# Performance work log

Measured on AMD Instinct MI355X. Metric: run time of the kernel, lower is better.

Reference implementation:

```python
import jax, jax.numpy as jnp
import numpy as np

N = 6144      # nodes
DIN = 65      # input_dim (1 time + 64 space coords)
DOUT = 65     # output_dim per head
H = 4         # nheads
EPS = 1e-7
MIN = 1e-15
# curvature c = 1 throughout (MultiHeadGraphAttentionLayer hardcodes curvature=1)

def arcosh(z):
    return jnp.log(z + jnp.sqrt(jnp.maximum(z * z - 1.0, 0.0)))

def hyp_proj(u):
    # project onto hyperboloid: recompute time coord
    y = u[..., 1:]
    t = jnp.sqrt(1.0 + jnp.sum(y * y, -1, keepdims=True))
    return jnp.concatenate([t, y], -1)

def expmap0(u):
    v = u[..., 1:]
    n = jnp.maximum(jnp.linalg.norm(v, axis=-1, keepdims=True), MIN)
    return jnp.concatenate([jnp.cosh(n), jnp.sinh(n) * v / n], -1)

def logmap0(x):
    y = x[..., 1:]
    n = jnp.maximum(jnp.linalg.norm(y, axis=-1, keepdims=True), MIN)
    t = jnp.maximum(x[..., :1], 1.0 + EPS)
    return jnp.concatenate([jnp.zeros_like(t), arcosh(t) * y / n], -1)

def hyp_linear(x, W):
    # HypLinear (use_bias=False, eval mode): mobius_matvec = exp0(log0(x) @ W^T), then proj
    return hyp_proj(expmap0(logmap0(x) @ W.T))

def to_poincare(x):
    return x[..., 1:] / (x[..., :1] + 1.0)

def to_hyperboloid(p):
    s = jnp.sum(p * p, -1, keepdims=True)
    return jnp.concatenate([1.0 + s, 2.0 * p], -1) / jnp.maximum(1.0 - s, MIN)

def mobius_half(v):
    # 0.5 (x) v  (mobius scalar multiplication, c=1)
    n = jnp.maximum(jnp.linalg.norm(v, axis=-1, keepdims=True), MIN)
    return jnp.tanh(0.5 * jnp.arctanh(jnp.minimum(n, 1.0 - EPS))) * v / n

def head(x, adj_t, Wa, Wd, Wo):
    att = hyp_linear(x, Wa)   # [N, DOUT]
    red = hyp_linear(x, Wd)   # [N, DOUT]
    # pairwise hyperboloid sqdist via Minkowski inner product (negate time coord)
    am = att.at[:, 0].multiply(-1.0)
    theta = jnp.maximum(-(am @ att.T), 1.0 + EPS)          # [N, N]
    S = jnp.minimum(arcosh(theta) ** 2, 50.0)
    # coef[i, j] = -adj[j, i] * sqdist for incoming edges (mask = adj^T)
    coef = jnp.where(adj_t > 0.01, -adj_t * S, 0.0)
    # F.normalize along incoming-edge axis (zeros don't change the L2 norm)
    a = coef / jnp.maximum(jnp.linalg.norm(coef, axis=-1, keepdims=True), 1e-12)
    pv = to_poincare(red)                                   # [N, DOUT-1]
    lam = 2.0 / jnp.maximum(1.0 - jnp.sum(pv * pv, -1), MIN)  # conformal factors [N]
    num = (a * lam[None, :]) @ pv                           # [N, DOUT-1]
    den = jnp.sum(jnp.abs(a) * (lam - 1.0)[None, :], -1, keepdims=True)
    m = mobius_half(num / jnp.maximum(den, MIN))            # mobius midpoint
    return hyp_linear(to_hyperboloid(m), Wo)                # [N, DOUT]

def reference(x, adj, W_att, W_data, W_out, W_lin):
    adj_t = adj.T
    hs = jnp.stack([head(x, adj_t, W_att[h], W_data[h], W_out[h]) for h in range(H)], axis=1)  # [N, H, DOUT]
    p = to_poincare(hs).reshape(x.shape[0], -1)             # PoincareBall.concat -> [N, H*(DOUT-1)]
    return hyp_linear(to_hyperboloid(p), W_lin)             # [N, H*DOUT]

def setup_inputs():
    key = jax.random.key(0)
    ks = jax.random.split(key, 8)
    sp = 0.1 * jax.random.normal(ks[0], (N, DIN - 1), jnp.float32)
    x = jnp.concatenate([jnp.sqrt(1.0 + jnp.sum(sp * sp, -1, keepdims=True)), sp], -1)
    adj = (jax.random.uniform(ks[1], (N, N)) < 32.0 / N).astype(jnp.float32)
    adj = jnp.maximum(adj, jnp.eye(N, dtype=jnp.float32))  # every node >=1 incoming edge
    def xavier(k, shape):
        b = (6.0 / (shape[0] + shape[1])) ** 0.5
        return jax.random.uniform(k, shape, jnp.float32, -b, b)
    W_att = jnp.stack([xavier(jax.random.fold_in(ks[2], h), (DOUT, DIN)) for h in range(H)])
    W_data = jnp.stack([xavier(jax.random.fold_in(ks[3], h), (DOUT, DIN)) for h in range(H)])
    W_out = jnp.stack([xavier(jax.random.fold_in(ks[4], h), (DOUT, DOUT)) for h in range(H)])
    W_lin = xavier(ks[5], (H * DOUT, H * (DOUT - 1) + 1))
    return {"x": x, "adj": adj, "W_att": W_att, "W_data": W_data, "W_out": W_out, "W_lin": W_lin}
```

## Files before the change

### kernel.cpp

```cpp
#include <hip/hip_runtime.h>
#include <math.h>

#define N 6144
#define H 4
#define CAP 128
#define MINF 1e-15f
#define ONE_EPS  1.0000001192092896f
#define ONE_MEPS 0.9999998807907104f

__device__ __forceinline__ float wave_reduce_sum(float v) {
    v += __shfl_xor(v, 32, 64);
    v += __shfl_xor(v, 16, 64);
    v += __shfl_xor(v, 8, 64);
    v += __shfl_xor(v, 4, 64);
    v += __shfl_xor(v, 2, 64);
    v += __shfl_xor(v, 1, 64);
    return v;
}

__device__ __forceinline__ float arcosh_f(float z) {
    return logf(z + sqrtf(fmaxf(z * z - 1.0f, 0.0f)));
}

__global__ void k_prep(const float* __restrict__ x, float* __restrict__ lmv,
                       const float* __restrict__ W_att, const float* __restrict__ W_data,
                       const float* __restrict__ W_out,
                       float* __restrict__ Bp, float* __restrict__ Bo,
                       int* __restrict__ cnt) {
    int b = blockIdx.x;
    if (b < 1536) {
        int i = b * 4 + (threadIdx.x >> 6);
        int lane = threadIdx.x & 63;
        float y = x[i * 65 + 1 + lane];
        float ss = wave_reduce_sum(y * y);
        float n = fmaxf(sqrtf(ss), MINF);
        float t = fmaxf(x[i * 65], ONE_EPS);
        lmv[i * 64 + lane] = arcosh_f(t) * y / n;
    } else if (b < 1728) {
        int tid = (b - 1536) * 256 + threadIdx.x;
        int m = tid >> 12;
        int r = tid & 4095;
        int k = r >> 6, o = r & 63;
        const float* src;
        if (m < 4) src = W_att + m * 65 * 65;
        else if (m < 8) src = W_data + (m - 4) * 65 * 65;
        else src = W_out + (m - 8) * 65 * 65;
        float val = src[(1 + o) * 65 + (1 + k)];
        if (m < 8) Bp[m * 4096 + k * 64 + o] = val;
        else Bo[(m - 8) * 4096 + k * 64 + o] = val;
    } else {
        cnt[(b - 1728) * 256 + threadIdx.x] = 0;
    }
}

__global__ void k_build_csr(const float* __restrict__ adj,
                            int* __restrict__ cnt, int* __restrict__ idx) {
    const unsigned total4 = (unsigned)N * N / 4;
    const float4* a4 = (const float4*)adj;
    for (unsigned e = blockIdx.x * blockDim.x + threadIdx.x; e < total4;
         e += gridDim.x * blockDim.x) {
        float4 v = a4[e];
        unsigned base = e * 4u;
        float vals[4] = {v.x, v.y, v.z, v.w};
        #pragma unroll
        for (int q = 0; q < 4; q++) {
            if (vals[q] > 0.01f) {
                unsigned t = base + q;
                int j = t / N;
                int i = t % N;
                int pos = atomicAdd(&cnt[i], 1);
                if (pos < CAP) idx[i * CAP + pos] = j;
            }
        }
    }
}

__global__ void k_gemm64(const float* __restrict__ A, size_t aStrideY,
                         const float* __restrict__ Bp, float* __restrict__ C, int ldc) {
    __shared__ float As[16][64];
    __shared__ float Bs[16][64];
    const float* Ab = A + aStrideY * blockIdx.y;
    const float* Bb = Bp + (size_t)blockIdx.y * 4096;
    int i0 = blockIdx.x * 64;
    int ocol = blockIdx.y * 64;
    int tid = threadIdx.x;
    int tx = tid & 15, ty = tid >> 4;
    float acc[4][4] = {};
    for (int k0 = 0; k0 < 64; k0 += 16) {
        {
            int mm = tid >> 2, kq = tid & 3;
            float4 v = *(const float4*)(Ab + (size_t)(i0 + mm) * 64 + k0 + kq * 4);
            As[kq * 4 + 0][mm] = v.x;
            As[kq * 4 + 1][mm] = v.y;
            As[kq * 4 + 2][mm] = v.z;
            As[kq * 4 + 3][mm] = v.w;
        }
        {
            int kk = tid >> 4, o4 = tid & 15;
            float4 bvv = *(const float4*)(Bb + (k0 + kk) * 64 + o4 * 4);
            *(float4*)&Bs[kk][o4 * 4] = bvv;
        }
        __syncthreads();
        #pragma unroll
        for (int kk = 0; kk < 16; kk++) {
            float4 av = *(const float4*)&As[kk][ty * 4];
            float4 bv = *(const float4*)&Bs[kk][tx * 4];
            float a[4] = {av.x, av.y, av.z, av.w};
            float b[4] = {bv.x, bv.y, bv.z, bv.w};
            #pragma unroll
            for (int r = 0; r < 4; r++)
                #pragma unroll
                for (int c = 0; c < 4; c++) acc[r][c] += a[r] * b[c];
        }
        __syncthreads();
    }
    #pragma unroll
    for (int r = 0; r < 4; r++) {
        int i = i0 + ty * 4 + r;
        #pragma unroll
        for (int c = 0; c < 4; c++)
            C[(size_t)i * ldc + ocol + tx * 4 + c] = acc[r][c];
    }
}

__global__ void k_head_epi(const float* __restrict__ UAUD,
                           float* __restrict__ attv, float2* __restrict__ a0l,
                           float* __restrict__ pv) {
    int i = blockIdx.x;
    int t = threadIdx.x;
    int h = t >> 6, lane = t & 63;
    float ua = UAUD[(size_t)i * 512 + t];
    float ud = UAUD[(size_t)i * 512 + 256 + t];
    float na = fmaxf(sqrtf(wave_reduce_sum(ua * ua)), MINF);
    float sha = sinhf(na);
    attv[((size_t)h * N + i) * 64 + lane] = sha * ua / na;
    float nd = fmaxf(sqrtf(wave_reduce_sum(ud * ud)), MINF);
    float shd = sinhf(nd), chd = coshf(nd);
    float pvd = (shd * ud / nd) / (chd + 1.0f);
    pv[((size_t)h * N + i) * 64 + lane] = pvd;
    float sp = wave_reduce_sum(pvd * pvd);
    if (lane == 0) {
        a0l[h * N + i] = make_float2(coshf(na), 2.0f / fmaxf(1.0f - sp, MINF));
    }
}

__global__ void __launch_bounds__(256) k_attn(
        const int* __restrict__ cnt, const int* __restrict__ idx,
        const float* __restrict__ attv, const float2* __restrict__ a0l,
        const float* __restrict__ pv, float* __restrict__ lm2) {
    __shared__ float wls[4][CAP];
    __shared__ int jls[4][CAP];
    int w = threadIdx.x >> 6, lane = threadIdx.x & 63;
    int i = blockIdx.x * 4 + w;
    int h = blockIdx.y;
    const float* attvh = attv + (size_t)h * N * 64;
    const float* pvh = pv + (size_t)h * N * 64;
    const float2* a0lh = a0l + (size_t)h * N;

    int c = lane & 3;
    float4 aireg[4];
    #pragma unroll
    for (int q = 0; q < 4; q++)
        aireg[q] = *(const float4*)(attvh + (size_t)i * 64 + q * 16 + c * 4);
    float ai0 = a0lh[i].x;
    int nn = min(cnt[i], CAP);

    float accd = 0.f, accss = 0.f;
    for (int base = 0; base < nn; base += 16) {
        int t = base + (lane >> 2);
        bool act = t < nn;
        int j = act ? idx[i * CAP + t] : i;
        float2 al = a0lh[j];
        float d = 0.f;
        #pragma unroll
        for (int q = 0; q < 4; q++) {
            float4 b = *(const float4*)(attvh + (size_t)j * 64 + q * 16 + c * 4);
            float4 a = aireg[q];
            d += a.x * b.x + a.y * b.y + a.z * b.z + a.w * b.w;
        }
        d += __shfl_xor(d, 1, 64);
        d += __shfl_xor(d, 2, 64);
        float theta = fmaxf(ai0 * al.x - d, ONE_EPS);
        float ar = arcosh_f(theta);
        float S = fminf(ar * ar, 50.0f);
        if (!act) S = 0.f;
        if (c == 0) {
            accd += S * (al.y - 1.0f);
            accss += S * S;
            wls[w][t] = S * al.y;
            jls[w][t] = j;
        }
    }
    accd = wave_reduce_sum(accd);
    accss = wave_reduce_sum(accss);
    float nrm = fmaxf(sqrtf(accss), 1e-12f);
    float den = fmaxf(accd / nrm, MINF);
    float scl = 1.0f / (nrm * den);

    float accn = 0.f;
    #pragma unroll 4
    for (int t = 0; t < nn; t++) {
        int j = jls[w][t];
        float wq = wls[w][t];
        accn = fmaf(wq, pvh[(size_t)j * 64 + lane], accn);
    }
    float v = -scl * accn;
    float nv = fmaxf(sqrtf(wave_reduce_sum(v * v)), MINF);
    float nc = fminf(nv, ONE_MEPS);
    float mh = tanhf(0.5f * atanhf(nc));
    float md = mh * v / nv;
    float s = wave_reduce_sum(md * md);
    float Dh = fmaxf(1.0f - s, MINF);
    float hb0 = (1.0f + s) / Dh;
    float hbv = 2.0f * md / Dh;
    float nh = fmaxf(2.0f * sqrtf(s) / Dh, MINF);
    float t2 = fmaxf(hb0, ONE_EPS);
    lm2[((size_t)h * N + i) * 64 + lane] = arcosh_f(t2) * hbv / nh;
}

__global__ void k_out_epi(const float* __restrict__ u2, float* __restrict__ lmF) {
    __shared__ float part[4];
    int i = blockIdx.x;
    int t = threadIdx.x;
    int w = t >> 6;
    float u = u2[(size_t)i * 256 + t];
    float nv = fmaxf(sqrtf(wave_reduce_sum(u * u)), MINF);
    float sh = sinhf(nv), ch = coshf(nv);
    float pd = (sh * u / nv) / (ch + 1.0f);
    float ss = wave_reduce_sum(pd * pd);
    if ((t & 63) == 0) part[w] = ss;
    __syncthreads();
    float s = part[0] + part[1] + part[2] + part[3];
    float Dh = fmaxf(1.0f - s, MINF);
    float hb0 = (1.0f + s) / Dh;
    float hbv = 2.0f * pd / Dh;
    float n = fmaxf(2.0f * sqrtf(s) / Dh, MINF);
    float tt = fmaxf(hb0, ONE_EPS);
    lmF[(size_t)i * 256 + t] = arcosh_f(tt) * hbv / n;
}

__global__ void k_final_gemm(const float* __restrict__ A,
                             const float* __restrict__ Wl,
                             float* __restrict__ U) {
    __shared__ float As[16][64];
    __shared__ float Bs[16][64];
    int i0 = blockIdx.x * 64;
    int o0 = blockIdx.y * 64;
    int tid = threadIdx.x;
    int tx = tid & 15, ty = tid >> 4;
    float acc[4][4] = {};
    for (int k0 = 0; k0 < 256; k0 += 16) {
        {
            int mm = tid >> 2;
            int kq = tid & 3;
            const float4 v = *(const float4*)(A + (size_t)(i0 + mm) * 256 + k0 + kq * 4);
            As[kq * 4 + 0][mm] = v.x;
            As[kq * 4 + 1][mm] = v.y;
            As[kq * 4 + 2][mm] = v.z;
            As[kq * 4 + 3][mm] = v.w;
        }
        {
            int oo = tid >> 2;
            int kq = tid & 3;
            int o = o0 + oo;
            if (o < 259) {
                const float* src = Wl + (size_t)(1 + o) * 257 + 1 + k0 + kq * 4;
                Bs[kq * 4 + 0][oo] = src[0];
                Bs[kq * 4 + 1][oo] = src[1];
                Bs[kq * 4 + 2][oo] = src[2];
                Bs[kq * 4 + 3][oo] = src[3];
            } else {
                Bs[kq * 4 + 0][oo] = 0.f;
                Bs[kq * 4 + 1][oo] = 0.f;
                Bs[kq * 4 + 2][oo] = 0.f;
                Bs[kq * 4 + 3][oo] = 0.f;
            }
        }
        __syncthreads();
        #pragma unroll
        for (int kk = 0; kk < 16; kk++) {
            float4 av = *(const float4*)&As[kk][ty * 4];
            float4 bv = *(const float4*)&Bs[kk][tx * 4];
            float a[4] = {av.x, av.y, av.z, av.w};
            float b[4] = {bv.x, bv.y, bv.z, bv.w};
            #pragma unroll
            for (int r = 0; r < 4; r++)
                #pragma unroll
                for (int c = 0; c < 4; c++) acc[r][c] += a[r] * b[c];
        }
        __syncthreads();
    }
    #pragma unroll
    for (int r = 0; r < 4; r++) {
        int i = i0 + ty * 4 + r;
        #pragma unroll
        for (int c = 0; c < 4; c++) {
            int o = o0 + tx * 4 + c;
            if (o < 259) U[(size_t)i * 260 + o] = acc[r][c];
        }
    }
}

__global__ void k_final_epilogue(const float* __restrict__ U, float* __restrict__ out) {
    __shared__ float part[4];
    int i = blockIdx.x;
    int t = threadIdx.x;
    float a = U[(size_t)i * 260 + t];
    float b = (t < 3) ? U[(size_t)i * 260 + 256 + t] : 0.f;
    float ss = wave_reduce_sum(a * a + b * b);
    if ((t & 63) == 0) part[t >> 6] = ss;
    __syncthreads();
    ss = part[0] + part[1] + part[2] + part[3];
    float nv = fmaxf(sqrtf(ss), MINF);
    float sh = sinhf(nv);
    float scale = sh / nv;
    out[(size_t)i * 260 + 1 + t] = scale * a;
    if (t < 3) out[(size_t)i * 260 + 257 + t] = scale * b;
    if (t == 0) out[(size_t)i * 260] = sqrtf(1.0f + sh * sh);
}

extern "C" void kernel_launch(void* const* d_in, const int* in_sizes, int n_in,
                              void* d_out, int out_size, void* d_ws, size_t ws_size,
                              hipStream_t stream) {
    const float* x = (const float*)d_in[0];
    const float* adj = (const float*)d_in[1];
    const float* W_att = (const float*)d_in[2];
    const float* W_data = (const float*)d_in[3];
    const float* W_out = (const float*)d_in[4];
    const float* W_lin = (const float*)d_in[5];
    float* out = (float*)d_out;

    char* ws = (char*)d_ws;
    size_t off = 0;
    auto alloc = [&](size_t bytes) {
        void* ptr = ws + off;
        off += (bytes + 255) & ~(size_t)255;
        return ptr;
    };
    int* cnt = (int*)alloc((size_t)N * 4);
    int* idx = (int*)alloc((size_t)N * CAP * 4);
    float* lmv = (float*)alloc((size_t)N * 64 * 4);
    float* UAUD = (float*)alloc((size_t)N * 512 * 4);
    float* attv = (float*)alloc((size_t)H * N * 64 * 4);
    float2* a0l = (float2*)alloc((size_t)H * N * 8);
    float* pvb = (float*)alloc((size_t)H * N * 64 * 4);
    float* lm2 = (float*)alloc((size_t)H * N * 64 * 4);
    float* Bp = (float*)alloc((size_t)8 * 4096 * 4);
    float* Bo = (float*)alloc((size_t)4 * 4096 * 4);
    float* U = UAUD;
    float* lmF = attv;
    float* u2 = pvb;

    k_prep<<<1752, 256, 0, stream>>>(x, lmv, W_att, W_data, W_out, Bp, Bo, cnt);
    k_build_csr<<<4096, 256, 0, stream>>>(adj, cnt, idx);
    k_gemm64<<<dim3(N / 64, 8), 256, 0, stream>>>(lmv, 0, Bp, UAUD, 512);
    k_head_epi<<<N, 256, 0, stream>>>(UAUD, attv, a0l, pvb);
    k_attn<<<dim3(N / 4, H), 256, 0, stream>>>(cnt, idx, attv, a0l, pvb, lm2);
    k_gemm64<<<dim3(N / 64, 4), 256, 0, stream>>>(lm2, (size_t)N * 64, Bo, u2, 256);
    k_out_epi<<<N, 256, 0, stream>>>(u2, lmF);
    k_final_gemm<<<dim3(N / 64, 5), 256, 0, stream>>>(lmF, W_lin, U);
    k_final_epilogue<<<N, 256, 0, stream>>>(U, out);
}
```

Baseline: 351.4 us.

## Fuse CSR build with head GEMM and fold epilogues into GEMM kernels

Merges the adjacency scan (CSR build) and the per-head projection GEMM into one launch, with block ranges split between the two tasks so they can run concurrently. The head epilogue (expmap and Poincaré conversion) moves into the GEMM via a shared-memory C tile, which removes the UAUD intermediate round trip. The output GEMM likewise absorbs the per-head expmap, leaving only the logmap in a separate kernel. In exchange the epilogue runs as a serial 16-row loop per wave, and the larger shared-memory footprint may lower occupancy.

```diff
diff --git a/kernel.cpp b/kernel.cpp
--- a/kernel.cpp
+++ b/kernel.cpp
@@ -53,94 +53,95 @@
     }
 }
 
-__global__ void k_build_csr(const float* __restrict__ adj,
-                            int* __restrict__ cnt, int* __restrict__ idx) {
-    const unsigned total4 = (unsigned)N * N / 4;
-    const float4* a4 = (const float4*)adj;
-    for (unsigned e = blockIdx.x * blockDim.x + threadIdx.x; e < total4;
-         e += gridDim.x * blockDim.x) {
-        float4 v = a4[e];
-        unsigned base = e * 4u;
-        float vals[4] = {v.x, v.y, v.z, v.w};
-        #pragma unroll
-        for (int q = 0; q < 4; q++) {
-            if (vals[q] > 0.01f) {
-                unsigned t = base + q;
-                int j = t / N;
-                int i = t % N;
-                int pos = atomicAdd(&cnt[i], 1);
-                if (pos < CAP) idx[i * CAP + pos] = j;
-            }
-        }
-    }
-}
-
-__global__ void k_gemm64(const float* __restrict__ A, size_t aStrideY,
-                         const float* __restrict__ Bp, float* __restrict__ C, int ldc) {
+__global__ void __launch_bounds__(256) k_csr_gemm(
+        const float* __restrict__ adj, int* __restrict__ cnt, int* __restrict__ idx,
+        const float* __restrict__ lmv, const float* __restrict__ Bp,
+        float* __restrict__ attv, float2* __restrict__ a0l, float* __restrict__ pv) {
     __shared__ float As[16][64];
     __shared__ float Bs[16][64];
-    const float* Ab = A + aStrideY * blockIdx.y;
-    const float* Bb = Bp + (size_t)blockIdx.y * 4096;
-    int i0 = blockIdx.x * 64;
-    int ocol = blockIdx.y * 64;
-    int tid = threadIdx.x;
-    int tx = tid & 15, ty = tid >> 4;
-    float acc[4][4] = {};
-    for (int k0 = 0; k0 < 64; k0 += 16) {
-        {
-            int mm = tid >> 2, kq = tid & 3;
-            float4 v = *(const float4*)(Ab + (size_t)(i0 + mm) * 64 + k0 + kq * 4);
-            As[kq * 4 + 0][mm] = v.x;
-            As[kq * 4 + 1][mm] = v.y;
-            As[kq * 4 + 2][mm] = v.z;
-            As[kq * 4 + 3][mm] = v.w;
-        }
-        {
-            int kk = tid >> 4, o4 = tid & 15;
-            float4 bvv = *(const float4*)(Bb + (k0 + kk) * 64 + o4 * 4);
-            *(float4*)&Bs[kk][o4 * 4] = bvv;
-        }
+    __shared__ float Cs[64][65];
+    if (blockIdx.x < 768) {
+        int my = blockIdx.x / 96;
+        int ix = blockIdx.x % 96;
+        const float* Bb = Bp + (size_t)my * 4096;
+        int i0 = ix * 64;
+        int tid = threadIdx.x;
+        int tx = tid & 15, ty = tid >> 4;
+        float acc[4][4] = {};
+        for (int k0 = 0; k0 < 64; k0 += 16) {
+            {
+                int mm = tid >> 2, kq = tid & 3;
+                float4 v = *(const float4*)(lmv + (size_t)(i0 + mm) * 64 + k0 + kq * 4);
+                As[kq * 4 + 0][mm] = v.x;
+                As[kq * 4 + 1][mm] = v.y;
+                As[kq * 4 + 2][mm] = v.z;
+                As[kq * 4 + 3][mm] = v.w;
+            }
+            {
+                int kk = tid >> 4, o4 = tid & 15;
+                float4 bvv = *(const float4*)(Bb + (k0 + kk) * 64 + o4 * 4);
+                *(float4*)&Bs[kk][o4 * 4] = bvv;
+            }
+            __syncthreads();
+            #pragma unroll
+            for (int kk = 0; kk < 16; kk++) {
+                float4 av = *(const float4*)&As[kk][ty * 4];
+                float4 bv = *(const float4*)&Bs[kk][tx * 4];
+                float a[4] = {av.x, av.y, av.z, av.w};
+                float b[4] = {bv.x, bv.y, bv.z, bv.w};
+                #pragma unroll
+                for (int r = 0; r < 4; r++)
+                    #pragma unroll
+                    for (int c = 0; c < 4; c++) acc[r][c] += a[r] * b[c];
+            }
+            __syncthreads();
+        }
+        #pragma unroll
+        for (int r = 0; r < 4; r++)
+            #pragma unroll
+            for (int c = 0; c < 4; c++)
+                Cs[ty * 4 + r][tx * 4 + c] = acc[r][c];
         __syncthreads();
-        #pragma unroll
-        for (int kk = 0; kk < 16; kk++) {
-            float4 av = *(const float4*)&As[kk][ty * 4];
-            float4 bv = *(const float4*)&Bs[kk][tx * 4];
-            float a[4] = {av.x, av.y, av.z, av.w};
-            float b[4] = {bv.x, bv.y, bv.z, bv.w};
+        int w = tid >> 6, lane = tid & 63;
+        int h = my & 3;
+        bool isAtt = my < 4;
+        #pragma unroll 1
+        for (int r16 = 0; r16 < 16; r16++) {
+            int row = w * 16 + r16;
+            int i = i0 + row;
+            float u = Cs[row][lane];
+            float nn = fmaxf(sqrtf(wave_reduce_sum(u * u)), MINF);
+            if (isAtt) {
+                float sha = sinhf(nn);
+                attv[((size_t)h * N + i) * 64 + lane] = sha * u / nn;
+                if (lane == 0) a0l[h * N + i].x = coshf(nn);
+            } else {
+                float shd = sinhf(nn), chd = coshf(nn);
+                float pvd = (shd * u / nn) / (chd + 1.0f);
+                pv[((size_t)h * N + i) * 64 + lane] = pvd;
+                float sp = wave_reduce_sum(pvd * pvd);
+                if (lane == 0) a0l[h * N + i].y = 2.0f / fmaxf(1.0f - sp, MINF);
+            }
+        }
+    } else {
+        const unsigned total4 = (unsigned)N * N / 4;
+        const float4* a4 = (const float4*)adj;
+        for (unsigned e = (blockIdx.x - 768) * 256 + threadIdx.x; e < total4;
+             e += 4096u * 256u) {
+            float4 v = a4[e];
+            unsigned base = e * 4u;
+            float vals[4] = {v.x, v.y, v.z, v.w};
             #pragma unroll
-            for (int r = 0; r < 4; r++)
-                #pragma unroll
-                for (int c = 0; c < 4; c++) acc[r][c] += a[r] * b[c];
-        }
-        __syncthreads();
-    }
-    #pragma unroll
-    for (int r = 0; r < 4; r++) {
-        int i = i0 + ty * 4 + r;
-        #pragma unroll
-        for (int c = 0; c < 4; c++)
-            C[(size_t)i * ldc + ocol + tx * 4 + c] = acc[r][c];
-    }
-}
-
-__global__ void k_head_epi(const float* __restrict__ UAUD,
-                           float* __restrict__ attv, float2* __restrict__ a0l,
-                           float* __restrict__ pv) {
-    int i = blockIdx.x;
-    int t = threadIdx.x;
-    int h = t >> 6, lane = t & 63;
-    float ua = UAUD[(size_t)i * 512 + t];
-    float ud = UAUD[(size_t)i * 512 + 256 + t];
-    float na = fmaxf(sqrtf(wave_reduce_sum(ua * ua)), MINF);
-    float sha = sinhf(na);
-    attv[((size_t)h * N + i) * 64 + lane] = sha * ua / na;
-    float nd = fmaxf(sqrtf(wave_reduce_sum(ud * ud)), MINF);
-    float shd = sinhf(nd), chd = coshf(nd);
-    float pvd = (shd * ud / nd) / (chd + 1.0f);
-    pv[((size_t)h * N + i) * 64 + lane] = pvd;
-    float sp = wave_reduce_sum(pvd * pvd);
-    if (lane == 0) {
-        a0l[h * N + i] = make_float2(coshf(na), 2.0f / fmaxf(1.0f - sp, MINF));
+            for (int q = 0; q < 4; q++) {
+                if (vals[q] > 0.01f) {
+                    unsigned t = base + q;
+                    int j = t / N;
+                    int i = t % N;
+                    int pos = atomicAdd(&cnt[i], 1);
+                    if (pos < CAP) idx[i * CAP + pos] = j;
+                }
+            }
+        }
     }
 }
 
@@ -218,15 +219,71 @@
     lm2[((size_t)h * N + i) * 64 + lane] = arcosh_f(t2) * hbv / nh;
 }
 
-__global__ void k_out_epi(const float* __restrict__ u2, float* __restrict__ lmF) {
+__global__ void __launch_bounds__(256) k_gemm_out(
+        const float* __restrict__ lm2, const float* __restrict__ Bo,
+        float* __restrict__ p) {
+    __shared__ float As[16][64];
+    __shared__ float Bs[16][64];
+    __shared__ float Cs[64][65];
+    int h = blockIdx.y;
+    const float* Ab = lm2 + (size_t)h * N * 64;
+    const float* Bb = Bo + (size_t)h * 4096;
+    int i0 = blockIdx.x * 64;
+    int tid = threadIdx.x;
+    int tx = tid & 15, ty = tid >> 4;
+    float acc[4][4] = {};
+    for (int k0 = 0; k0 < 64; k0 += 16) {
+        {
+            int mm = tid >> 2, kq = tid & 3;
+            float4 v = *(const float4*)(Ab + (size_t)(i0 + mm) * 64 + k0 + kq * 4);
+            As[kq * 4 + 0][mm] = v.x;
+            As[kq * 4 + 1][mm] = v.y;
+            As[kq * 4 + 2][mm] = v.z;
+            As[kq * 4 + 3][mm] = v.w;
+        }
+        {
+            int kk = tid >> 4, o4 = tid & 15;
+            float4 bvv = *(const float4*)(Bb + (k0 + kk) * 64 + o4 * 4);
+            *(float4*)&Bs[kk][o4 * 4] = bvv;
+        }
+        __syncthreads();
+        #pragma unroll
+        for (int kk = 0; kk < 16; kk++) {
+            float4 av = *(const float4*)&As[kk][ty * 4];
+            float4 bv = *(const float4*)&Bs[kk][tx * 4];
+            float a[4] = {av.x, av.y, av.z, av.w};
+            float b[4] = {bv.x, bv.y, bv.z, bv.w};
+            #pragma unroll
+            for (int r = 0; r < 4; r++)
+                #pragma unroll
+                for (int c = 0; c < 4; c++) acc[r][c] += a[r] * b[c];
+        }
+        __syncthreads();
+    }
+    #pragma unroll
+    for (int r = 0; r < 4; r++)
+        #pragma unroll
+        for (int c = 0; c < 4; c++)
+            Cs[ty * 4 + r][tx * 4 + c] = acc[r][c];
+    __syncthreads();
+    int w = tid >> 6, lane = tid & 63;
+    #pragma unroll 1
+    for (int r16 = 0; r16 < 16; r16++) {
+        int row = w * 16 + r16;
+        int i = i0 + row;
+        float u = Cs[row][lane];
+        float nv = fmaxf(sqrtf(wave_reduce_sum(u * u)), MINF);
+        float sh = sinhf(nv), ch = coshf(nv);
+        p[(size_t)i * 256 + h * 64 + lane] = (sh * u / nv) / (ch + 1.0f);
+    }
+}
+
+__global__ void k_final_logmap(const float* __restrict__ p, float* __restrict__ lmF) {
     __shared__ float part[4];
     int i = blockIdx.x;
     int t = threadIdx.x;
     int w = t >> 6;
-    float u = u2[(size_t)i * 256 + t];
-    float nv = fmaxf(sqrtf(wave_reduce_sum(u * u)), MINF);
-    float sh = sinhf(nv), ch = coshf(nv);
-    float pd = (sh * u / nv) / (ch + 1.0f);
+    float pd = p[(size_t)i * 256 + t];
     float ss = wave_reduce_sum(pd * pd);
     if ((t & 63) == 0) part[w] = ss;
     __syncthreads();
@@ -340,24 +397,21 @@
     int* cnt = (int*)alloc((size_t)N * 4);
     int* idx = (int*)alloc((size_t)N * CAP * 4);
     float* lmv = (float*)alloc((size_t)N * 64 * 4);
-    float* UAUD = (float*)alloc((size_t)N * 512 * 4);
     float* attv = (float*)alloc((size_t)H * N * 64 * 4);
     float2* a0l = (float2*)alloc((size_t)H * N * 8);
     float* pvb = (float*)alloc((size_t)H * N * 64 * 4);
     float* lm2 = (float*)alloc((size_t)H * N * 64 * 4);
+    float* U = (float*)alloc((size_t)N * 260 * 4);
     float* Bp = (float*)alloc((size_t)8 * 4096 * 4);
     float* Bo = (float*)alloc((size_t)4 * 4096 * 4);
-    float* U = UAUD;
     float* lmF = attv;
-    float* u2 = pvb;
+    float* p = pvb;
 
     k_prep<<<1752, 256, 0, stream>>>(x, lmv, W_att, W_data, W_out, Bp, Bo, cnt);
-    k_build_csr<<<4096, 256, 0, stream>>>(adj, cnt, idx);
-    k_gemm64<<<dim3(N / 64, 8), 256, 0, stream>>>(lmv, 0, Bp, UAUD, 512);
-    k_head_epi<<<N, 256, 0, stream>>>(UAUD, attv, a0l, pvb);
+    k_csr_gemm<<<4864, 256, 0, stream>>>(adj, cnt, idx, lmv, Bp, attv, a0l, pvb);
     k_attn<<<dim3(N / 4, H), 256, 0, stream>>>(cnt, idx, attv, a0l, pvb, lm2);
-    k_gemm64<<<dim3(N / 64, 4), 256, 0, stream>>>(lm2, (size_t)N * 64, Bo, u2, 256);
-    k_out_epi<<<N, 256, 0, stream>>>(u2, lmF);
+    k_gemm_out<<<dim3(N / 64, H), 256, 0, stream>>>(lm2, Bo, p);
+    k_final_logmap<<<N, 256, 0, stream>>>(p, lmF);
     k_final_gemm<<<dim3(N / 64, 5), 256, 0, stream>>>(lmF, W_lin, U);
     k_final_epilogue<<<N, 256, 0, stream>>>(U, out);
 }
```

Measured after the change: 349.2 us. About the same (-0.6%).
